# Performance work log

Hardware: AMD Instinct MI355X
Metric: run time of the kernel (lower is better)

Reference implementation:

```python
import jax, jax.numpy as jnp
import numpy as np

C = 64          # num_channels
DEPTH = 9       # dilation_depth
REPEAT = 2      # dilation_repeat
K = 2           # kernel_size
DILATIONS = [2 ** j for _ in range(REPEAT) for j in range(DEPTH)]
L = len(DILATIONS)  # 18 gated layers


def causal_conv(x, w, b, dilation):
    # x: [B, Cin, T], w: [Cout, Cin, K] -> [B, Cout, T] with causal (left) padding
    pad = (w.shape[-1] - 1) * dilation
    y = jax.lax.conv_general_dilated(
        x, w, window_strides=(1,), padding=[(pad, 0)],
        rhs_dilation=(dilation,), dimension_numbers=("NCH", "OIH", "NCH"))
    return y + b[None, :, None]


def setup_inputs() -> dict:
    key = jax.random.key(0)
    ks = jax.random.split(key, 9)
    s = 0.1
    x = jax.random.normal(ks[0], (4, 1, 65536), dtype=jnp.float32)
    in_w = jax.random.normal(ks[1], (C, 1, 1), dtype=jnp.float32) * s
    in_b = jax.random.normal(ks[2], (C,), dtype=jnp.float32) * s
    hid_w = jax.random.normal(ks[3], (L, 2 * C, C, K), dtype=jnp.float32) * s
    hid_b = jax.random.normal(ks[4], (L, 2 * C), dtype=jnp.float32) * s
    res_w = jax.random.normal(ks[5], (L, C, C, 1), dtype=jnp.float32) * s
    res_b = jax.random.normal(ks[6], (L, C), dtype=jnp.float32) * s
    mix_w = jax.random.normal(ks[7], (1, C * L, 1), dtype=jnp.float32) * s
    mix_b = jax.random.normal(ks[8], (1,), dtype=jnp.float32) * s
    return {"x": x, "in_w": in_w, "in_b": in_b, "hid_w": hid_w, "hid_b": hid_b,
            "res_w": res_w, "res_b": res_b, "mix_w": mix_w, "mix_b": mix_b}


def reference(x, in_w, in_b, hid_w, hid_b, res_w, res_b, mix_w, mix_b):
    # Input 1x1 conv: [B,1,T] -> [B,C,T]
    out = causal_conv(x, in_w, in_b, 1)
    skips = []
    for i, d in enumerate(DILATIONS):
        xi = out
        h = causal_conv(xi, hid_w[i], hid_b[i], d)       # [B, 2C, T]
        gated = jnp.tanh(h[:, :C]) * jax.nn.sigmoid(h[:, C:])  # [B, C, T]
        skips.append(gated)
        out = causal_conv(gated, res_w[i], res_b[i], 1) + xi    # residual
    skip = jnp.concatenate(skips, axis=1)                # [B, C*L, T]
    return causal_conv(skip, mix_w, mix_b, 1)            # [B, 1, T]
```

## Files before the change

### kernel.cpp

```cpp
#include <hip/hip_runtime.h>
#include <hip/hip_bf16.h>
#include <math.h>

#define NCH 64
#define T_LEN 65536
#define NLAYER 18

typedef __attribute__((ext_vector_type(8))) short bf16x8;
typedef __attribute__((ext_vector_type(4))) short bf16x4;
typedef __attribute__((ext_vector_type(4))) float f32x4;

static __device__ __forceinline__ float bf2f(short s) {
    union { short u[2]; float f; } v;
    v.u[0] = 0; v.u[1] = s;
    return v.f;
}
static __device__ __forceinline__ short f2bf(float f) {
    __hip_bfloat16 h = __float2bfloat16(f);
    return *(short*)&h;
}

__global__ void convert_weights_kernel(const float* __restrict__ hid_w,
                                       const float* __restrict__ res_w,
                                       __hip_bfloat16* __restrict__ whid,
                                       __hip_bfloat16* __restrict__ wres) {
    int gid = blockIdx.x * 256 + threadIdx.x;
    if (gid < NLAYER * 128 * 128) {
        int l   = gid >> 14;
        int rem = gid & 16383;
        int o   = rem >> 7;
        int k   = rem & 127;
        float v = (k < 64)
            ? hid_w[((l * 128 + o) * 64 + k) * 2]
            : hid_w[((l * 128 + o) * 64 + (k - 64)) * 2 + 1];
        whid[gid] = __float2bfloat16(v);
    }
    if (gid < NLAYER * 64 * 64) {
        wres[gid] = __float2bfloat16(res_w[gid]);
    }
}

__global__ __launch_bounds__(256, 3) void fused6_kernel(
    const void* __restrict__ src,
    __hip_bfloat16* __restrict__ next,
    float* __restrict__ acc,
    const __hip_bfloat16* __restrict__ whid_all,
    const float* __restrict__ hb_all,
    const __hip_bfloat16* __restrict__ wres_all,
    const float* __restrict__ rb_all,
    const float* __restrict__ mix_w,
    const float* __restrict__ in_w,
    const float* __restrict__ in_b,
    int lbase, int is_first) {
    __shared__ __align__(16) __hip_bfloat16 A[192 * 64];
    __shared__ __align__(16) __hip_bfloat16 G[192 * 64];

#define SW(row, col) ((row) * 64 + ((col) ^ (((row) & 7) << 3)))

    const int b    = blockIdx.x >> 9;
    const int widx = blockIdx.x & 511;
    const int t0   = widx << 7;
    const int tw   = t0 - 64;

    const int tid  = threadIdx.x;
    const int lane = tid & 63;
    const int w4   = tid >> 6;
    const int l15  = lane & 15;
    const int quad = lane >> 4;
    const int m0   = w4 * 16;
    const int rr   = tid >> 3;
    const int co   = (tid & 7) * 8;

    if (is_first) {
        const float* x = (const float*)src;
        float iw[8], ib[8];
#pragma unroll
        for (int j = 0; j < 8; ++j) { iw[j] = in_w[co + j]; ib[j] = in_b[co + j]; }
#pragma unroll
        for (int round = 0; round < 6; ++round) {
            int r  = round * 32 + rr;
            int gt = tw + r;
            bf16x8 v = {0, 0, 0, 0, 0, 0, 0, 0};
            if (gt >= 0) {
                float xv = x[(size_t)b * T_LEN + gt];
#pragma unroll
                for (int j = 0; j < 8; ++j) v[j] = f2bf(iw[j] * xv + ib[j]);
            }
            *(bf16x8*)(&A[SW(r, co)]) = v;
        }
    } else {
        const __hip_bfloat16* prev = (const __hip_bfloat16*)src;
#pragma unroll
        for (int round = 0; round < 6; ++round) {
            int r  = round * 32 + rr;
            int gt = tw + r;
            bf16x8 v = {0, 0, 0, 0, 0, 0, 0, 0};
            if (gt >= 0)
                v = *(const bf16x8*)(prev + ((size_t)b * T_LEN + gt) * NCH + co);
            *(bf16x8*)(&A[SW(r, co)]) = v;
        }
    }

    float skp[8] = {0.f, 0.f, 0.f, 0.f, 0.f, 0.f, 0.f, 0.f};

#pragma unroll 1
    for (int l = 0; l < 6; ++l) {
        const int d = 1 << l;
        const __hip_bfloat16* whid = whid_all + (size_t)(lbase + l) * 16384;
        const __hip_bfloat16* wres = wres_all + (size_t)(lbase + l) * 4096;
        const float* hb = hb_all + (lbase + l) * 128;
        const float* rb = rb_all + (lbase + l) * 64;
        const float* mw = mix_w + (lbase + l) * 64;

        bf16x8 aT[4], aS[4], aR[2];
        {
            const __hip_bfloat16* whT = whid + (size_t)(m0 + l15) * 128 + quad * 8;
            const __hip_bfloat16* whS = whT + 64 * 128;
#pragma unroll
            for (int k = 0; k < 4; ++k) {
                aT[k] = *(const bf16x8*)(whT + k * 32);
                aS[k] = *(const bf16x8*)(whS + k * 32);
            }
            const __hip_bfloat16* wrA = wres + (size_t)(m0 + l15) * 64 + quad * 8;
            aR[0] = *(const bf16x8*)(wrA);
            aR[1] = *(const bf16x8*)(wrA + 32);
        }
        f32x4 biasT, biasS, biasR;
#pragma unroll
        for (int r = 0; r < 4; ++r) {
            biasT[r] = hb[m0 + quad * 4 + r];
            biasS[r] = hb[64 + m0 + quad * 4 + r];
            biasR[r] = rb[m0 + quad * 4 + r];
        }
        f32x4 mw4 = *(const f32x4*)(mw + m0 + quad * 4);

        __syncthreads();

#pragma unroll
        for (int ct = 0; ct < 3; ++ct) {
            f32x4 accT[4], accS[4];
#pragma unroll
            for (int nt = 0; nt < 4; ++nt) { accT[nt] = biasT; accS[nt] = biasS; }
#pragma unroll
            for (int ks = 0; ks < 4; ++ks) {
                const int koff = (ks & 1) * 32 + quad * 8;
#pragma unroll
                for (int nt = 0; nt < 4; ++nt) {
                    int trow = ct * 64 + nt * 16 + l15;
                    int prow = trow - d;  prow = prow < 0 ? 0 : prow;
                    int row  = (ks < 2) ? prow : trow;
                    bf16x8 bx = *(const bf16x8*)(&A[SW(row, koff)]);
                    accT[nt] = __builtin_amdgcn_mfma_f32_16x16x32_bf16(aT[ks], bx, accT[nt], 0, 0, 0);
                    accS[nt] = __builtin_amdgcn_mfma_f32_16x16x32_bf16(aS[ks], bx, accS[nt], 0, 0, 0);
                }
            }
#pragma unroll
            for (int nt = 0; nt < 4; ++nt) {
                int trow = ct * 64 + nt * 16 + l15;
                bf16x4 gv;
                float gsum = 0.f;
#pragma unroll
                for (int r = 0; r < 4; ++r) {
                    float ea = __expf(2.f * accT[nt][r]);
                    float eb = __expf(-accS[nt][r]);
                    float g  = (ea - 1.f) *
                               __builtin_amdgcn_rcpf((ea + 1.f) * (1.f + eb));
                    gsum += mw4[r] * g;
                    gv[r] = f2bf(g);
                }
                if (ct >= 1) skp[(ct - 1) * 4 + nt] += gsum;
                *(bf16x4*)(&G[SW(trow, m0 + quad * 4)]) = gv;
            }
        }
        __syncthreads();

#pragma unroll
        for (int ct = 0; ct < 3; ++ct) {
            f32x4 accR[4];
#pragma unroll
            for (int nt = 0; nt < 4; ++nt) accR[nt] = biasR;
#pragma unroll
            for (int ks = 0; ks < 2; ++ks) {
                const int koff = ks * 32 + quad * 8;
#pragma unroll
                for (int nt = 0; nt < 4; ++nt) {
                    int trow = ct * 64 + nt * 16 + l15;
                    bf16x8 bx = *(const bf16x8*)(&G[SW(trow, koff)]);
                    accR[nt] = __builtin_amdgcn_mfma_f32_16x16x32_bf16(aR[ks], bx, accR[nt], 0, 0, 0);
                }
            }
#pragma unroll
            for (int nt = 0; nt < 4; ++nt) {
                int trow = ct * 64 + nt * 16 + l15;
                bf16x4 old = *(const bf16x4*)(&A[SW(trow, m0 + quad * 4)]);
                bool ok = (tw + trow) >= 0;
                bf16x4 ov;
#pragma unroll
                for (int r = 0; r < 4; ++r) {
                    float v = accR[nt][r] + bf2f(old[r]);
                    ov[r] = f2bf(ok ? v : 0.f);
                }
                *(bf16x4*)(&A[SW(trow, m0 + quad * 4)]) = ov;
            }
        }
    }
    __syncthreads();

#pragma unroll
    for (int round = 0; round < 4; ++round) {
        int pr = round * 32 + rr;
        *(bf16x8*)(next + ((size_t)b * T_LEN + t0 + pr) * NCH + co) =
            *(const bf16x8*)(&A[SW(pr + 64, co)]);
    }

    float* skbuf = (float*)G;
#pragma unroll
    for (int i = 0; i < 8; ++i) {
        skp[i] += __shfl_xor(skp[i], 16, 64);
        skp[i] += __shfl_xor(skp[i], 32, 64);
    }
    if (quad == 0) {
#pragma unroll
        for (int i = 0; i < 8; ++i) {
            int ct = i >> 2, nt = i & 3;
            skbuf[w4 * 128 + ct * 64 + nt * 16 + l15] = skp[i];
        }
    }
    __syncthreads();
    if (tid < 128) {
        float tot = skbuf[tid] + skbuf[128 + tid] +
                    skbuf[256 + tid] + skbuf[384 + tid];
        acc[(size_t)b * T_LEN + t0 + tid] += tot;
    }
#undef SW
}

__global__ __launch_bounds__(256, 2) void layer_mfma_kernel(
    const __hip_bfloat16* __restrict__ prev,
    __hip_bfloat16* __restrict__ next,
    float* __restrict__ acc,
    const __hip_bfloat16* __restrict__ whid,
    const float* __restrict__ hb,
    const __hip_bfloat16* __restrict__ wres,
    const float* __restrict__ rb,
    const float* __restrict__ mw,
    int d) {
    __shared__ __align__(16) __hip_bfloat16 Xp[64 * 72];
    __shared__ __align__(16) __hip_bfloat16 Xc[64 * 72];
    __shared__ __align__(16) __hip_bfloat16 Gt[64 * 72];

    const int t0   = blockIdx.x << 6;
    const int tid  = threadIdx.x;
    const int lane = tid & 63;
    const int w4   = tid >> 6;
    const int l15  = lane & 15;
    const int quad = lane >> 4;
    const int m0   = w4 * 16;
    const int rr = tid >> 3;
    const int co = (tid & 7) * 8;

    bf16x8 aT[4], aS[4], aR[2];
    {
        const __hip_bfloat16* whT = whid + (size_t)(m0 + l15) * 128 + quad * 8;
        const __hip_bfloat16* whS = whT + 64 * 128;
#pragma unroll
        for (int k = 0; k < 4; ++k) {
            aT[k] = *(const bf16x8*)(whT + k * 32);
            aS[k] = *(const bf16x8*)(whS + k * 32);
        }
        const __hip_bfloat16* wrA = wres + (size_t)(m0 + l15) * 64 + quad * 8;
        aR[0] = *(const bf16x8*)(wrA);
        aR[1] = *(const bf16x8*)(wrA + 32);
    }
    f32x4 biasT, biasS, biasR;
#pragma unroll
    for (int r = 0; r < 4; ++r) {
        biasT[r] = hb[m0 + quad * 4 + r];
        biasS[r] = hb[64 + m0 + quad * 4 + r];
        biasR[r] = rb[m0 + quad * 4 + r];
    }
    float mwq[16];
#pragma unroll
    for (int j = 0; j < 16; ++j) mwq[j] = mw[quad * 16 + j];

    bf16x8 pc[2], pp[2];
#define LOAD_TILE(b)                                                          \
    do {                                                                      \
        const __hip_bfloat16* pb = prev + ((size_t)(b) * T_LEN + t0) * NCH;   \
        _Pragma("unroll")                                                     \
        for (int pass = 0; pass < 2; ++pass) {                                \
            int r = pass * 32 + rr;                                           \
            pc[pass] = *(const bf16x8*)(pb + r * NCH + co);                   \
            int tp = t0 + r - d;                                              \
            bf16x8 z = {0, 0, 0, 0, 0, 0, 0, 0};                              \
            pp[pass] = z;                                                     \
            if (tp >= 0)                                                      \
                pp[pass] = *(const bf16x8*)(prev +                            \
                    ((size_t)(b) * T_LEN + tp) * NCH + co);                   \
        }                                                                     \
    } while (0)

    LOAD_TILE(0);

#pragma unroll
    for (int b = 0; b < 4; ++b) {
#pragma unroll
        for (int pass = 0; pass < 2; ++pass) {
            int r = pass * 32 + rr;
            *(bf16x8*)(&Xc[r * 72 + co]) = pc[pass];
            *(bf16x8*)(&Xp[r * 72 + co]) = pp[pass];
        }
        __syncthreads();

        if (b < 3) LOAD_TILE(b + 1);

        f32x4 accT[4], accS[4];
#pragma unroll
        for (int nt = 0; nt < 4; ++nt) { accT[nt] = biasT; accS[nt] = biasS; }
#pragma unroll
        for (int ks = 0; ks < 4; ++ks) {
            const __hip_bfloat16* srcb = (ks < 2) ? Xp : Xc;
            const int kk = (ks & 1) * 32 + quad * 8;
#pragma unroll
            for (int nt = 0; nt < 4; ++nt) {
                bf16x8 bx = *(const bf16x8*)(&srcb[(nt * 16 + l15) * 72 + kk]);
                accT[nt] = __builtin_amdgcn_mfma_f32_16x16x32_bf16(aT[ks], bx, accT[nt], 0, 0, 0);
                accS[nt] = __builtin_amdgcn_mfma_f32_16x16x32_bf16(aS[ks], bx, accS[nt], 0, 0, 0);
            }
        }

#pragma unroll
        for (int nt = 0; nt < 4; ++nt) {
            int t = nt * 16 + l15;
#pragma unroll
            for (int r = 0; r < 4; ++r) {
                float e2 = __expf(2.f * accT[nt][r]);
                float th = 1.f - 2.f * __builtin_amdgcn_rcpf(e2 + 1.f);
                float sg = __builtin_amdgcn_rcpf(1.f + __expf(-accS[nt][r]));
                Gt[t * 72 + m0 + quad * 4 + r] = __float2bfloat16(th * sg);
            }
        }

        bf16x4 curres[4];
#pragma unroll
        for (int nt = 0; nt < 4; ++nt) {
            curres[nt] = *(const bf16x4*)(&Xc[(nt * 16 + l15) * 72 + m0 + quad * 4]);
        }
        __syncthreads();

        f32x4 accR[4];
#pragma unroll
        for (int nt = 0; nt < 4; ++nt) accR[nt] = biasR;
#pragma unroll
        for (int ks = 0; ks < 2; ++ks) {
            const int kk = ks * 32 + quad * 8;
#pragma unroll
            for (int nt = 0; nt < 4; ++nt) {
                bf16x8 bx = *(const bf16x8*)(&Gt[(nt * 16 + l15) * 72 + kk]);
                accR[nt] = __builtin_amdgcn_mfma_f32_16x16x32_bf16(aR[ks], bx, accR[nt], 0, 0, 0);
            }
        }

        __hip_bfloat16* nb = next + ((size_t)b * T_LEN + t0) * NCH;
#pragma unroll
        for (int nt = 0; nt < 4; ++nt) {
            int t = nt * 16 + l15;
            bf16x4 ov;
#pragma unroll
            for (int r = 0; r < 4; ++r) {
                ov[r] = f2bf(accR[nt][r] + bf2f(curres[nt][r]));
            }
            *(bf16x4*)(nb + t * NCH + m0 + quad * 4) = ov;
        }

        {
            int t = w4 * 16 + l15;
            bf16x8 g0 = *(const bf16x8*)(&Gt[t * 72 + quad * 16]);
            bf16x8 g1 = *(const bf16x8*)(&Gt[t * 72 + quad * 16 + 8]);
            float s = 0.f;
#pragma unroll
            for (int j = 0; j < 8; ++j) {
                s += mwq[j]     * bf2f(g0[j]);
                s += mwq[8 + j] * bf2f(g1[j]);
            }
            s += __shfl_xor(s, 16, 64);
            s += __shfl_xor(s, 32, 64);
            if (quad == 0)
                acc[(size_t)b * T_LEN + t0 + t] += s;
        }
    }
#undef LOAD_TILE
}

__global__ __launch_bounds__(256, 2) void last_layer_kernel(
    const __hip_bfloat16* __restrict__ prev,
    const float* __restrict__ acc,
    float* __restrict__ out,
    const __hip_bfloat16* __restrict__ whid,
    const float* __restrict__ hb,
    const float* __restrict__ mw,
    const float* __restrict__ mix_b,
    int d) {
    __shared__ __align__(16) __hip_bfloat16 Xp[64 * 72];
    __shared__ __align__(16) __hip_bfloat16 Xc[64 * 72];
    __shared__ float skb[4 * 64];

    const int t0   = blockIdx.x << 6;
    const int tid  = threadIdx.x;
    const int lane = tid & 63;
    const int w4   = tid >> 6;
    const int l15  = lane & 15;
    const int quad = lane >> 4;
    const int m0   = w4 * 16;
    const int rr = tid >> 3;
    const int co = (tid & 7) * 8;

    bf16x8 aT[4], aS[4];
    {
        const __hip_bfloat16* whT = whid + (size_t)(m0 + l15) * 128 + quad * 8;
        const __hip_bfloat16* whS = whT + 64 * 128;
#pragma unroll
        for (int k = 0; k < 4; ++k) {
            aT[k] = *(const bf16x8*)(whT + k * 32);
            aS[k] = *(const bf16x8*)(whS + k * 32);
        }
    }
    f32x4 biasT, biasS;
    float mwv[4];
#pragma unroll
    for (int r = 0; r < 4; ++r) {
        biasT[r] = hb[m0 + quad * 4 + r];
        biasS[r] = hb[64 + m0 + quad * 4 + r];
        mwv[r]   = mw[m0 + quad * 4 + r];
    }
    const float mb = mix_b[0];

    bf16x8 pc[2], pp[2];
#define LOAD_TILE(b)                                                          \
    do {                                                                      \
        const __hip_bfloat16* pb = prev + ((size_t)(b) * T_LEN + t0) * NCH;   \
        _Pragma("unroll")                                                     \
        for (int pass = 0; pass < 2; ++pass) {                                \
            int r = pass * 32 + rr;                                           \
            pc[pass] = *(const bf16x8*)(pb + r * NCH + co);                   \
            int tp = t0 + r - d;                                              \
            bf16x8 z = {0, 0, 0, 0, 0, 0, 0, 0};                              \
            pp[pass] = z;                                                     \
            if (tp >= 0)                                                      \
                pp[pass] = *(const bf16x8*)(prev +                            \
                    ((size_t)(b) * T_LEN + tp) * NCH + co);                   \
        }                                                                     \
    } while (0)

    LOAD_TILE(0);

#pragma unroll
    for (int b = 0; b < 4; ++b) {
#pragma unroll
        for (int pass = 0; pass < 2; ++pass) {
            int r = pass * 32 + rr;
            *(bf16x8*)(&Xc[r * 72 + co]) = pc[pass];
            *(bf16x8*)(&Xp[r * 72 + co]) = pp[pass];
        }
        __syncthreads();

        if (b < 3) LOAD_TILE(b + 1);

        f32x4 accT[4], accS[4];
#pragma unroll
        for (int nt = 0; nt < 4; ++nt) { accT[nt] = biasT; accS[nt] = biasS; }
#pragma unroll
        for (int ks = 0; ks < 4; ++ks) {
            const __hip_bfloat16* srcb = (ks < 2) ? Xp : Xc;
            const int kk = (ks & 1) * 32 + quad * 8;
#pragma unroll
            for (int nt = 0; nt < 4; ++nt) {
                bf16x8 bx = *(const bf16x8*)(&srcb[(nt * 16 + l15) * 72 + kk]);
                accT[nt] = __builtin_amdgcn_mfma_f32_16x16x32_bf16(aT[ks], bx, accT[nt], 0, 0, 0);
                accS[nt] = __builtin_amdgcn_mfma_f32_16x16x32_bf16(aS[ks], bx, accS[nt], 0, 0, 0);
            }
        }

#pragma unroll
        for (int nt = 0; nt < 4; ++nt) {
            float sv = 0.f;
#pragma unroll
            for (int r = 0; r < 4; ++r) {
                float e2 = __expf(2.f * accT[nt][r]);
                float th = 1.f - 2.f * __builtin_amdgcn_rcpf(e2 + 1.f);
                float sg = __builtin_amdgcn_rcpf(1.f + __expf(-accS[nt][r]));
                sv += mwv[r] * (th * sg);
            }
            sv += __shfl_xor(sv, 16, 64);
            sv += __shfl_xor(sv, 32, 64);
            if (quad == 0)
                skb[w4 * 64 + nt * 16 + l15] = sv;
        }
        __syncthreads();

        if (tid < 64) {
            float tot = skb[tid] + skb[64 + tid] + skb[128 + tid] + skb[192 + tid];
            out[(size_t)b * T_LEN + t0 + tid] =
                acc[(size_t)b * T_LEN + t0 + tid] + tot + mb;
        }
    }
#undef LOAD_TILE
}

extern "C" void kernel_launch(void* const* d_in, const int* in_sizes, int n_in,
                              void* d_out, int out_size, void* d_ws, size_t ws_size,
                              hipStream_t stream) {
    const float* x     = (const float*)d_in[0];
    const float* in_w  = (const float*)d_in[1];
    const float* in_b  = (const float*)d_in[2];
    const float* hid_w = (const float*)d_in[3];
    const float* hid_b = (const float*)d_in[4];
    const float* res_w = (const float*)d_in[5];
    const float* res_b = (const float*)d_in[6];
    const float* mix_w = (const float*)d_in[7];
    const float* mix_b = (const float*)d_in[8];
    float* out = (float*)d_out;

    const size_t act_elems = 4ull * T_LEN * NCH;
    __hip_bfloat16* actA = (__hip_bfloat16*)d_ws;
    __hip_bfloat16* actB = actA + act_elems;
    float* acc = (float*)(actB + act_elems);
    __hip_bfloat16* whid = (__hip_bfloat16*)(acc + 4ull * T_LEN);
    __hip_bfloat16* wres = whid + (size_t)NLAYER * 128 * 128;

    hipMemsetAsync(acc, 0, 4ull * T_LEN * sizeof(float), stream);

    convert_weights_kernel<<<1152, 256, 0, stream>>>(hid_w, res_w, whid, wres);

    fused6_kernel<<<2048, 256, 0, stream>>>(
        x, actA, acc, whid, hid_b, wres, res_b, mix_w, in_w, in_b, 0, 1);

    layer_mfma_kernel<<<1024, 256, 0, stream>>>(
        actA, actB, acc, whid + 6 * 16384, hid_b + 6 * 128,
        wres + 6 * 4096, res_b + 6 * 64, mix_w + 6 * 64, 64);
    layer_mfma_kernel<<<1024, 256, 0, stream>>>(
        actB, actA, acc, whid + 7 * 16384, hid_b + 7 * 128,
        wres + 7 * 4096, res_b + 7 * 64, mix_w + 7 * 64, 128);
    layer_mfma_kernel<<<1024, 256, 0, stream>>>(
        actA, actB, acc, whid + 8 * 16384, hid_b + 8 * 128,
        wres + 8 * 4096, res_b + 8 * 64, mix_w + 8 * 64, 256);

    fused6_kernel<<<2048, 256, 0, stream>>>(
        actB, actA, acc, whid, hid_b, wres, res_b, mix_w, in_w, in_b, 9, 0);

    layer_mfma_kernel<<<1024, 256, 0, stream>>>(
        actA, actB, acc, whid + 15 * 16384, hid_b + 15 * 128,
        wres + 15 * 4096, res_b + 15 * 64, mix_w + 15 * 64, 64);
    layer_mfma_kernel<<<1024, 256, 0, stream>>>(
        actB, actA, acc, whid + 16 * 16384, hid_b + 16 * 128,
        wres + 16 * 4096, res_b + 16 * 64, mix_w + 16 * 64, 128);

    last_layer_kernel<<<1024, 256, 0, stream>>>(
        actA, acc, out, whid + 17 * 16384, hid_b + 17 * 128,
        mix_w + 17 * 64, mix_b, 256);
}
```

Measured before the change: 530.4 us.

## Split fused6 work across 8 waves and raise occupancy bounds on layer kernels

The fused six-layer kernel now runs 512 threads per block. Each of 8 waves covers a 16-channel group for half of the 192 time rows, so it holds 3 accumulator tiles per chunk instead of 4 tiles over 3 chunks. This lowers per-wave register pressure and doubles the waves available to hide LDS and MFMA latency for the same shared-memory tile. The skip-sum bookkeeping is remapped to match. Separately, launch bounds on layer_mfma_kernel and last_layer_kernel are raised to 4 blocks per CU, which may force register spills.

After: 1.245 ms. 2.35x slower.

```diff
diff --git a/kernel.cpp b/kernel.cpp
--- a/kernel.cpp
+++ b/kernel.cpp
@@ -40,7 +40,7 @@
     }
 }
 
-__global__ __launch_bounds__(256, 3) void fused6_kernel(
+__global__ __launch_bounds__(512, 6) void fused6_kernel(
     const void* __restrict__ src,
     __hip_bfloat16* __restrict__ next,
     float* __restrict__ acc,
@@ -64,10 +64,13 @@
 
     const int tid  = threadIdx.x;
     const int lane = tid & 63;
-    const int w4   = tid >> 6;
+    const int w8   = tid >> 6;
+    const int rh   = w8 >> 2;
+    const int cg   = w8 & 3;
     const int l15  = lane & 15;
     const int quad = lane >> 4;
-    const int m0   = w4 * 16;
+    const int m0   = cg * 16;
+    const int rbase = rh * 96;
     const int rr   = tid >> 3;
     const int co   = (tid & 7) * 8;
 
@@ -77,8 +80,8 @@
 #pragma unroll
         for (int j = 0; j < 8; ++j) { iw[j] = in_w[co + j]; ib[j] = in_b[co + j]; }
 #pragma unroll
-        for (int round = 0; round < 6; ++round) {
-            int r  = round * 32 + rr;
+        for (int round = 0; round < 3; ++round) {
+            int r  = round * 64 + rr;
             int gt = tw + r;
             bf16x8 v = {0, 0, 0, 0, 0, 0, 0, 0};
             if (gt >= 0) {
@@ -91,8 +94,8 @@
     } else {
         const __hip_bfloat16* prev = (const __hip_bfloat16*)src;
 #pragma unroll
-        for (int round = 0; round < 6; ++round) {
-            int r  = round * 32 + rr;
+        for (int round = 0; round < 3; ++round) {
+            int r  = round * 64 + rr;
             int gt = tw + r;
             bf16x8 v = {0, 0, 0, 0, 0, 0, 0, 0};
             if (gt >= 0)
@@ -101,7 +104,7 @@
         }
     }
 
-    float skp[8] = {0.f, 0.f, 0.f, 0.f, 0.f, 0.f, 0.f, 0.f};
+    float skp[6] = {0.f, 0.f, 0.f, 0.f, 0.f, 0.f};
 
 #pragma unroll 1
     for (int l = 0; l < 6; ++l) {
@@ -137,16 +140,16 @@
         __syncthreads();
 
 #pragma unroll
-        for (int ct = 0; ct < 3; ++ct) {
-            f32x4 accT[4], accS[4];
-#pragma unroll
-            for (int nt = 0; nt < 4; ++nt) { accT[nt] = biasT; accS[nt] = biasS; }
+        for (int ch = 0; ch < 2; ++ch) {
+            f32x4 accT[3], accS[3];
+#pragma unroll
+            for (int nt = 0; nt < 3; ++nt) { accT[nt] = biasT; accS[nt] = biasS; }
 #pragma unroll
             for (int ks = 0; ks < 4; ++ks) {
                 const int koff = (ks & 1) * 32 + quad * 8;
 #pragma unroll
-                for (int nt = 0; nt < 4; ++nt) {
-                    int trow = ct * 64 + nt * 16 + l15;
+                for (int nt = 0; nt < 3; ++nt) {
+                    int trow = rbase + ch * 48 + nt * 16 + l15;
                     int prow = trow - d;  prow = prow < 0 ? 0 : prow;
                     int row  = (ks < 2) ? prow : trow;
                     bf16x8 bx = *(const bf16x8*)(&A[SW(row, koff)]);
@@ -155,8 +158,8 @@
                 }
             }
 #pragma unroll
-            for (int nt = 0; nt < 4; ++nt) {
-                int trow = ct * 64 + nt * 16 + l15;
+            for (int nt = 0; nt < 3; ++nt) {
+                int trow = rbase + ch * 48 + nt * 16 + l15;
                 bf16x4 gv;
                 float gsum = 0.f;
 #pragma unroll
@@ -168,30 +171,31 @@
                     gsum += mw4[r] * g;
                     gv[r] = f2bf(g);
                 }
-                if (ct >= 1) skp[(ct - 1) * 4 + nt] += gsum;
+                if (rh == 1 || ch * 48 + nt * 16 >= 64)
+                    skp[ch * 3 + nt] += gsum;
                 *(bf16x4*)(&G[SW(trow, m0 + quad * 4)]) = gv;
             }
         }
         __syncthreads();
 
 #pragma unroll
-        for (int ct = 0; ct < 3; ++ct) {
-            f32x4 accR[4];
-#pragma unroll
-            for (int nt = 0; nt < 4; ++nt) accR[nt] = biasR;
+        for (int ch = 0; ch < 2; ++ch) {
+            f32x4 accR[3];
+#pragma unroll
+            for (int nt = 0; nt < 3; ++nt) accR[nt] = biasR;
 #pragma unroll
             for (int ks = 0; ks < 2; ++ks) {
                 const int koff = ks * 32 + quad * 8;
 #pragma unroll
-                for (int nt = 0; nt < 4; ++nt) {
-                    int trow = ct * 64 + nt * 16 + l15;
+                for (int nt = 0; nt < 3; ++nt) {
+                    int trow = rbase + ch * 48 + nt * 16 + l15;
                     bf16x8 bx = *(const bf16x8*)(&G[SW(trow, koff)]);
                     accR[nt] = __builtin_amdgcn_mfma_f32_16x16x32_bf16(aR[ks], bx, accR[nt], 0, 0, 0);
                 }
             }
 #pragma unroll
-            for (int nt = 0; nt < 4; ++nt) {
-                int trow = ct * 64 + nt * 16 + l15;
+            for (int nt = 0; nt < 3; ++nt) {
+                int trow = rbase + ch * 48 + nt * 16 + l15;
                 bf16x4 old = *(const bf16x4*)(&A[SW(trow, m0 + quad * 4)]);
                 bool ok = (tw + trow) >= 0;
                 bf16x4 ov;
@@ -207,23 +211,28 @@
     __syncthreads();
 
 #pragma unroll
-    for (int round = 0; round < 4; ++round) {
-        int pr = round * 32 + rr;
+    for (int round = 0; round < 2; ++round) {
+        int pr = round * 64 + rr;
         *(bf16x8*)(next + ((size_t)b * T_LEN + t0 + pr) * NCH + co) =
             *(const bf16x8*)(&A[SW(pr + 64, co)]);
     }
 
     float* skbuf = (float*)G;
 #pragma unroll
-    for (int i = 0; i < 8; ++i) {
+    for (int i = 0; i < 6; ++i) {
         skp[i] += __shfl_xor(skp[i], 16, 64);
         skp[i] += __shfl_xor(skp[i], 32, 64);
     }
     if (quad == 0) {
 #pragma unroll
-        for (int i = 0; i < 8; ++i) {
-            int ct = i >> 2, nt = i & 3;
-            skbuf[w4 * 128 + ct * 64 + nt * 16 + l15] = skp[i];
+        for (int ch = 0; ch < 2; ++ch) {
+#pragma unroll
+            for (int nt = 0; nt < 3; ++nt) {
+                if (rh == 1 || ch * 48 + nt * 16 >= 64) {
+                    int row = rbase + ch * 48 + nt * 16 + l15 - 64;
+                    skbuf[cg * 128 + row] = skp[ch * 3 + nt];
+                }
+            }
         }
     }
     __syncthreads();
@@ -235,7 +244,7 @@
 #undef SW
 }
 
-__global__ __launch_bounds__(256, 2) void layer_mfma_kernel(
+__global__ __launch_bounds__(256, 4) void layer_mfma_kernel(
     const __hip_bfloat16* __restrict__ prev,
     __hip_bfloat16* __restrict__ next,
     float* __restrict__ acc,
@@ -392,7 +401,7 @@
 #undef LOAD_TILE
 }
 
-__global__ __launch_bounds__(256, 2) void last_layer_kernel(
+__global__ __launch_bounds__(256, 4) void last_layer_kernel(
     const __hip_bfloat16* __restrict__ prev,
     const float* __restrict__ acc,
     float* __restrict__ out,
@@ -532,7 +541,7 @@
 
     convert_weights_kernel<<<1152, 256, 0, stream>>>(hid_w, res_w, whid, wres);
 
-    fused6_kernel<<<2048, 256, 0, stream>>>(
+    fused6_kernel<<<2048, 512, 0, stream>>>(
         x, actA, acc, whid, hid_b, wres, res_b, mix_w, in_w, in_b, 0, 1);
 
     layer_mfma_kernel<<<1024, 256, 0, stream>>>(
@@ -545,7 +554,7 @@
         actA, actB, acc, whid + 8 * 16384, hid_b + 8 * 128,
         wres + 8 * 4096, res_b + 8 * 64, mix_w + 8 * 64, 256);
 
-    fused6_kernel<<<2048, 256, 0, stream>>>(
+    fused6_kernel<<<2048, 512, 0, stream>>>(
         actB, actA, acc, whid, hid_b, wres, res_b, mix_w, in_w, in_b, 9, 0);
 
     layer_mfma_kernel<<<1024, 256, 0, stream>>>(
```

## Double-buffer gate tile and interleave gated and residual GEMMs per chunk

Applied to the files above, without the earlier changes.

The full 192-row gate buffer in the fused six-layer kernel is replaced by two 64-row slots. The gated GEMM for one 64-row chunk is now interleaved with the residual GEMM of the previous chunk, and residual writes back into A are deferred past barriers to avoid read/write hazards. The smaller shared-memory footprint allows the launch bound to rise from 3 to 4 blocks per CU, aiming at more latency hiding. In exchange, more values stay live in registers (saved old activations and epilogue tiles) under a tighter per-thread register budget, which could cause spills.

Result: slower. 718.2 us (+35.4%).

```diff
diff --git a/kernel.cpp b/kernel.cpp
--- a/kernel.cpp
+++ b/kernel.cpp
@@ -40,7 +40,7 @@
     }
 }
 
-__global__ __launch_bounds__(256, 3) void fused6_kernel(
+__global__ __launch_bounds__(256, 4) void fused6_kernel(
     const void* __restrict__ src,
     __hip_bfloat16* __restrict__ next,
     float* __restrict__ acc,
@@ -53,7 +53,7 @@
     const float* __restrict__ in_b,
     int lbase, int is_first) {
     __shared__ __align__(16) __hip_bfloat16 A[192 * 64];
-    __shared__ __align__(16) __hip_bfloat16 G[192 * 64];
+    __shared__ __align__(16) __hip_bfloat16 Gb[2][64 * 64];
 
 #define SW(row, col) ((row) * 64 + ((col) ^ (((row) & 7) << 3)))
 
@@ -103,6 +103,72 @@
 
     float skp[8] = {0.f, 0.f, 0.f, 0.f, 0.f, 0.f, 0.f, 0.f};
 
+#define GEMM1_GATE(ct, slot)                                                  \
+    do {                                                                      \
+        f32x4 accT[4], accS[4];                                               \
+        _Pragma("unroll")                                                     \
+        for (int nt = 0; nt < 4; ++nt) { accT[nt] = biasT; accS[nt] = biasS; }\
+        _Pragma("unroll")                                                     \
+        for (int ks = 0; ks < 4; ++ks) {                                      \
+            const int koff = (ks & 1) * 32 + quad * 8;                        \
+            _Pragma("unroll")                                                 \
+            for (int nt = 0; nt < 4; ++nt) {                                  \
+                int trow = (ct) * 64 + nt * 16 + l15;                         \
+                int prow = trow - d;  prow = prow < 0 ? 0 : prow;             \
+                int row  = (ks < 2) ? prow : trow;                            \
+                bf16x8 bx = *(const bf16x8*)(&A[SW(row, koff)]);              \
+                accT[nt] = __builtin_amdgcn_mfma_f32_16x16x32_bf16(           \
+                    aT[ks], bx, accT[nt], 0, 0, 0);                           \
+                accS[nt] = __builtin_amdgcn_mfma_f32_16x16x32_bf16(           \
+                    aS[ks], bx, accS[nt], 0, 0, 0);                           \
+            }                                                                 \
+        }                                                                     \
+        _Pragma("unroll")                                                     \
+        for (int nt = 0; nt < 4; ++nt) {                                      \
+            bf16x4 gv;                                                        \
+            float gsum = 0.f;                                                 \
+            _Pragma("unroll")                                                 \
+            for (int r = 0; r < 4; ++r) {                                     \
+                float ea = __expf(2.f * accT[nt][r]);                         \
+                float eb = __expf(-accS[nt][r]);                              \
+                float g  = (ea - 1.f) *                                       \
+                           __builtin_amdgcn_rcpf((ea + 1.f) * (1.f + eb));    \
+                gsum += mw4[r] * g;                                           \
+                gv[r] = f2bf(g);                                              \
+            }                                                                 \
+            if ((ct) >= 1) skp[((ct) - 1) * 4 + nt] += gsum;                  \
+            *(bf16x4*)(&Gb[slot][SW(nt * 16 + l15, m0 + quad * 4)]) = gv;     \
+        }                                                                     \
+    } while (0)
+
+#define GEMM2_EPI(ct, slot, aold, epi)                                        \
+    do {                                                                      \
+        f32x4 accR[4];                                                        \
+        _Pragma("unroll")                                                     \
+        for (int nt = 0; nt < 4; ++nt) accR[nt] = biasR;                      \
+        _Pragma("unroll")                                                     \
+        for (int ks = 0; ks < 2; ++ks) {                                      \
+            const int koff = ks * 32 + quad * 8;                              \
+            _Pragma("unroll")                                                 \
+            for (int nt = 0; nt < 4; ++nt) {                                  \
+                bf16x8 bx =                                                   \
+                    *(const bf16x8*)(&Gb[slot][SW(nt * 16 + l15, koff)]);     \
+                accR[nt] = __builtin_amdgcn_mfma_f32_16x16x32_bf16(           \
+                    aR[ks], bx, accR[nt], 0, 0, 0);                           \
+            }                                                                 \
+        }                                                                     \
+        _Pragma("unroll")                                                     \
+        for (int nt = 0; nt < 4; ++nt) {                                      \
+            int trow = (ct) * 64 + nt * 16 + l15;                             \
+            bool ok = (tw + trow) >= 0;                                       \
+            _Pragma("unroll")                                                 \
+            for (int r = 0; r < 4; ++r) {                                     \
+                float v = accR[nt][r] + bf2f(aold[nt][r]);                    \
+                epi[nt][r] = f2bf(ok ? v : 0.f);                              \
+            }                                                                 \
+        }                                                                     \
+    } while (0)
+
 #pragma unroll 1
     for (int l = 0; l < 6; ++l) {
         const int d = 1 << l;
@@ -136,72 +202,39 @@
 
         __syncthreads();
 
-#pragma unroll
-        for (int ct = 0; ct < 3; ++ct) {
-            f32x4 accT[4], accS[4];
-#pragma unroll
-            for (int nt = 0; nt < 4; ++nt) { accT[nt] = biasT; accS[nt] = biasS; }
-#pragma unroll
-            for (int ks = 0; ks < 4; ++ks) {
-                const int koff = (ks & 1) * 32 + quad * 8;
-#pragma unroll
-                for (int nt = 0; nt < 4; ++nt) {
-                    int trow = ct * 64 + nt * 16 + l15;
-                    int prow = trow - d;  prow = prow < 0 ? 0 : prow;
-                    int row  = (ks < 2) ? prow : trow;
-                    bf16x8 bx = *(const bf16x8*)(&A[SW(row, koff)]);
-                    accT[nt] = __builtin_amdgcn_mfma_f32_16x16x32_bf16(aT[ks], bx, accT[nt], 0, 0, 0);
-                    accS[nt] = __builtin_amdgcn_mfma_f32_16x16x32_bf16(aS[ks], bx, accS[nt], 0, 0, 0);
-                }
-            }
-#pragma unroll
-            for (int nt = 0; nt < 4; ++nt) {
-                int trow = ct * 64 + nt * 16 + l15;
-                bf16x4 gv;
-                float gsum = 0.f;
-#pragma unroll
-                for (int r = 0; r < 4; ++r) {
-                    float ea = __expf(2.f * accT[nt][r]);
-                    float eb = __expf(-accS[nt][r]);
-                    float g  = (ea - 1.f) *
-                               __builtin_amdgcn_rcpf((ea + 1.f) * (1.f + eb));
-                    gsum += mw4[r] * g;
-                    gv[r] = f2bf(g);
-                }
-                if (ct >= 1) skp[(ct - 1) * 4 + nt] += gsum;
-                *(bf16x4*)(&G[SW(trow, m0 + quad * 4)]) = gv;
-            }
-        }
-        __syncthreads();
-
-#pragma unroll
-        for (int ct = 0; ct < 3; ++ct) {
-            f32x4 accR[4];
-#pragma unroll
-            for (int nt = 0; nt < 4; ++nt) accR[nt] = biasR;
-#pragma unroll
-            for (int ks = 0; ks < 2; ++ks) {
-                const int koff = ks * 32 + quad * 8;
-#pragma unroll
-                for (int nt = 0; nt < 4; ++nt) {
-                    int trow = ct * 64 + nt * 16 + l15;
-                    bf16x8 bx = *(const bf16x8*)(&G[SW(trow, koff)]);
-                    accR[nt] = __builtin_amdgcn_mfma_f32_16x16x32_bf16(aR[ks], bx, accR[nt], 0, 0, 0);
-                }
-            }
-#pragma unroll
-            for (int nt = 0; nt < 4; ++nt) {
-                int trow = ct * 64 + nt * 16 + l15;
-                bf16x4 old = *(const bf16x4*)(&A[SW(trow, m0 + quad * 4)]);
-                bool ok = (tw + trow) >= 0;
-                bf16x4 ov;
-#pragma unroll
-                for (int r = 0; r < 4; ++r) {
-                    float v = accR[nt][r] + bf2f(old[r]);
-                    ov[r] = f2bf(ok ? v : 0.f);
-                }
-                *(bf16x4*)(&A[SW(trow, m0 + quad * 4)]) = ov;
-            }
+        GEMM1_GATE(0, 0);
+        __syncthreads();
+
+        bf16x4 aold0[4], aold2[4], epi0[4];
+        GEMM1_GATE(1, 1);
+#pragma unroll
+        for (int nt = 0; nt < 4; ++nt) {
+            aold0[nt] = *(const bf16x4*)(&A[SW(nt * 16 + l15, m0 + quad * 4)]);
+            aold2[nt] = *(const bf16x4*)(&A[SW(128 + nt * 16 + l15, m0 + quad * 4)]);
+        }
+        GEMM2_EPI(0, 0, aold0, epi0);
+        __syncthreads();
+
+#pragma unroll
+        for (int nt = 0; nt < 4; ++nt)
+            *(bf16x4*)(&A[SW(nt * 16 + l15, m0 + quad * 4)]) = epi0[nt];
+        {
+            bf16x4 aold1[4], epi1[4];
+            GEMM1_GATE(2, 0);
+#pragma unroll
+            for (int nt = 0; nt < 4; ++nt)
+                aold1[nt] = *(const bf16x4*)(&A[SW(64 + nt * 16 + l15, m0 + quad * 4)]);
+            GEMM2_EPI(1, 1, aold1, epi1);
+            __syncthreads();
+
+#pragma unroll
+            for (int nt = 0; nt < 4; ++nt)
+                *(bf16x4*)(&A[SW(64 + nt * 16 + l15, m0 + quad * 4)]) = epi1[nt];
+            bf16x4 epi2[4];
+            GEMM2_EPI(2, 0, aold2, epi2);
+#pragma unroll
+            for (int nt = 0; nt < 4; ++nt)
+                *(bf16x4*)(&A[SW(128 + nt * 16 + l15, m0 + quad * 4)]) = epi2[nt];
         }
     }
     __syncthreads();
@@ -213,7 +246,7 @@
             *(const bf16x8*)(&A[SW(pr + 64, co)]);
     }
 
-    float* skbuf = (float*)G;
+    float* skbuf = (float*)Gb;
 #pragma unroll
     for (int i = 0; i < 8; ++i) {
         skp[i] += __shfl_xor(skp[i], 16, 64);
@@ -233,6 +266,8 @@
         acc[(size_t)b * T_LEN + t0 + tid] += tot;
     }
 #undef SW
+#undef GEMM1_GATE
+#undef GEMM2_EPI
 }
 
 __global__ __launch_bounds__(256, 2) void layer_mfma_kernel(
```

## Cut register pressure in layer kernel to raise occupancy to three blocks

Applied to the files above, without the earlier changes.

The per-layer MFMA kernel now targets three blocks per CU instead of two. It removes the register prefetch of the next batch tile, splits the gated-conv accumulation into two halves of two N-tiles each, and reloads residual weights and bias per batch iteration instead of keeping them resident. The skip-sum now comes from the fp32 gate values times per-row mix weights, reduced across waves through a small shared buffer, rather than re-reading bf16 gates from LDS. The tanh·sigmoid is also merged to use a single reciprocal. In exchange, it gives up overlap of global loads with compute, adds repeated weight loads, and adds an extra shared-memory stage.

Result: no change. 528.5 us (-0.4%).

```diff
diff --git a/kernel.cpp b/kernel.cpp
--- a/kernel.cpp
+++ b/kernel.cpp
@@ -235,7 +235,7 @@
 #undef SW
 }
 
-__global__ __launch_bounds__(256, 2) void layer_mfma_kernel(
+__global__ __launch_bounds__(256, 3) void layer_mfma_kernel(
     const __hip_bfloat16* __restrict__ prev,
     __hip_bfloat16* __restrict__ next,
     float* __restrict__ acc,
@@ -248,6 +248,7 @@
     __shared__ __align__(16) __hip_bfloat16 Xp[64 * 72];
     __shared__ __align__(16) __hip_bfloat16 Xc[64 * 72];
     __shared__ __align__(16) __hip_bfloat16 Gt[64 * 72];
+    __shared__ float skb[4 * 64];
 
     const int t0   = blockIdx.x << 6;
     const int tid  = threadIdx.x;
@@ -259,7 +260,7 @@
     const int rr = tid >> 3;
     const int co = (tid & 7) * 8;
 
-    bf16x8 aT[4], aS[4], aR[2];
+    bf16x8 aT[4], aS[4];
     {
         const __hip_bfloat16* whT = whid + (size_t)(m0 + l15) * 128 + quad * 8;
         const __hip_bfloat16* whS = whT + 64 * 128;
@@ -268,20 +269,170 @@
             aT[k] = *(const bf16x8*)(whT + k * 32);
             aS[k] = *(const bf16x8*)(whS + k * 32);
         }
-        const __hip_bfloat16* wrA = wres + (size_t)(m0 + l15) * 64 + quad * 8;
-        aR[0] = *(const bf16x8*)(wrA);
-        aR[1] = *(const bf16x8*)(wrA + 32);
-    }
-    f32x4 biasT, biasS, biasR;
+    }
+    f32x4 biasT, biasS;
 #pragma unroll
     for (int r = 0; r < 4; ++r) {
         biasT[r] = hb[m0 + quad * 4 + r];
         biasS[r] = hb[64 + m0 + quad * 4 + r];
-        biasR[r] = rb[m0 + quad * 4 + r];
-    }
-    float mwq[16];
-#pragma unroll
-    for (int j = 0; j < 16; ++j) mwq[j] = mw[quad * 16 + j];
+    }
+    f32x4 mw4 = *(const f32x4*)(mw + m0 + quad * 4);
+
+#pragma unroll 1
+    for (int b = 0; b < 4; ++b) {
+        {
+            const __hip_bfloat16* pb = prev + ((size_t)b * T_LEN + t0) * NCH;
+#pragma unroll
+            for (int pass = 0; pass < 2; ++pass) {
+                int r = pass * 32 + rr;
+                bf16x8 vc = *(const bf16x8*)(pb + r * NCH + co);
+                int tp = t0 + r - d;
+                bf16x8 vp = {0, 0, 0, 0, 0, 0, 0, 0};
+                if (tp >= 0)
+                    vp = *(const bf16x8*)(prev + ((size_t)b * T_LEN + tp) * NCH + co);
+                *(bf16x8*)(&Xc[r * 72 + co]) = vc;
+                *(bf16x8*)(&Xp[r * 72 + co]) = vp;
+            }
+        }
+        __syncthreads();
+
+        float sk[4];
+#pragma unroll
+        for (int np = 0; np < 2; ++np) {
+            f32x4 accT[2], accS[2];
+#pragma unroll
+            for (int h = 0; h < 2; ++h) { accT[h] = biasT; accS[h] = biasS; }
+#pragma unroll
+            for (int ks = 0; ks < 4; ++ks) {
+                const __hip_bfloat16* srcb = (ks < 2) ? Xp : Xc;
+                const int kk = (ks & 1) * 32 + quad * 8;
+#pragma unroll
+                for (int h = 0; h < 2; ++h) {
+                    int nt = np * 2 + h;
+                    bf16x8 bx = *(const bf16x8*)(&srcb[(nt * 16 + l15) * 72 + kk]);
+                    accT[h] = __builtin_amdgcn_mfma_f32_16x16x32_bf16(aT[ks], bx, accT[h], 0, 0, 0);
+                    accS[h] = __builtin_amdgcn_mfma_f32_16x16x32_bf16(aS[ks], bx, accS[h], 0, 0, 0);
+                }
+            }
+#pragma unroll
+            for (int h = 0; h < 2; ++h) {
+                int nt = np * 2 + h;
+                float gsum = 0.f;
+#pragma unroll
+                for (int r = 0; r < 4; ++r) {
+                    float ea = __expf(2.f * accT[h][r]);
+                    float eb = __expf(-accS[h][r]);
+                    float g  = (ea - 1.f) *
+                               __builtin_amdgcn_rcpf((ea + 1.f) * (1.f + eb));
+                    gsum += mw4[r] * g;
+                    Gt[(nt * 16 + l15) * 72 + m0 + quad * 4 + r] = __float2bfloat16(g);
+                }
+                sk[nt] = gsum;
+            }
+        }
+#pragma unroll
+        for (int nt = 0; nt < 4; ++nt) {
+            sk[nt] += __shfl_xor(sk[nt], 16, 64);
+            sk[nt] += __shfl_xor(sk[nt], 32, 64);
+        }
+        if (quad == 0) {
+#pragma unroll
+            for (int nt = 0; nt < 4; ++nt)
+                skb[w4 * 64 + nt * 16 + l15] = sk[nt];
+        }
+
+        bf16x4 curres[4];
+#pragma unroll
+        for (int nt = 0; nt < 4; ++nt) {
+            curres[nt] = *(const bf16x4*)(&Xc[(nt * 16 + l15) * 72 + m0 + quad * 4]);
+        }
+        __syncthreads();
+
+        bf16x8 aR0, aR1;
+        {
+            const __hip_bfloat16* wrA = wres + (size_t)(m0 + l15) * 64 + quad * 8;
+            aR0 = *(const bf16x8*)(wrA);
+            aR1 = *(const bf16x8*)(wrA + 32);
+        }
+        f32x4 biasR;
+#pragma unroll
+        for (int r = 0; r < 4; ++r) biasR[r] = rb[m0 + quad * 4 + r];
+
+        f32x4 accR[4];
+#pragma unroll
+        for (int nt = 0; nt < 4; ++nt) accR[nt] = biasR;
+#pragma unroll
+        for (int ks = 0; ks < 2; ++ks) {
+            const int kk = ks * 32 + quad * 8;
+#pragma unroll
+            for (int nt = 0; nt < 4; ++nt) {
+                bf16x8 bx = *(const bf16x8*)(&Gt[(nt * 16 + l15) * 72 + kk]);
+                accR[nt] = __builtin_amdgcn_mfma_f32_16x16x32_bf16(
+                    (ks == 0) ? aR0 : aR1, bx, accR[nt], 0, 0, 0);
+            }
+        }
+
+        __hip_bfloat16* nb = next + ((size_t)b * T_LEN + t0) * NCH;
+#pragma unroll
+        for (int nt = 0; nt < 4; ++nt) {
+            int t = nt * 16 + l15;
+            bf16x4 ov;
+#pragma unroll
+            for (int r = 0; r < 4; ++r) {
+                ov[r] = f2bf(accR[nt][r] + bf2f(curres[nt][r]));
+            }
+            *(bf16x4*)(nb + t * NCH + m0 + quad * 4) = ov;
+        }
+
+        if (tid < 64) {
+            float tot = skb[tid] + skb[64 + tid] + skb[128 + tid] + skb[192 + tid];
+            acc[(size_t)b * T_LEN + t0 + tid] += tot;
+        }
+    }
+}
+
+__global__ __launch_bounds__(256, 2) void last_layer_kernel(
+    const __hip_bfloat16* __restrict__ prev,
+    const float* __restrict__ acc,
+    float* __restrict__ out,
+    const __hip_bfloat16* __restrict__ whid,
+    const float* __restrict__ hb,
+    const float* __restrict__ mw,
+    const float* __restrict__ mix_b,
+    int d) {
+    __shared__ __align__(16) __hip_bfloat16 Xp[64 * 72];
+    __shared__ __align__(16) __hip_bfloat16 Xc[64 * 72];
+    __shared__ float skb[4 * 64];
+
+    const int t0   = blockIdx.x << 6;
+    const int tid  = threadIdx.x;
+    const int lane = tid & 63;
+    const int w4   = tid >> 6;
+    const int l15  = lane & 15;
+    const int quad = lane >> 4;
+    const int m0   = w4 * 16;
+    const int rr = tid >> 3;
+    const int co = (tid & 7) * 8;
+
+    bf16x8 aT[4], aS[4];
+    {
+        const __hip_bfloat16* whT = whid + (size_t)(m0 + l15) * 128 + quad * 8;
+        const __hip_bfloat16* whS = whT + 64 * 128;
+#pragma unroll
+        for (int k = 0; k < 4; ++k) {
+            aT[k] = *(const bf16x8*)(whT + k * 32);
+            aS[k] = *(const bf16x8*)(whS + k * 32);
+        }
+    }
+    f32x4 biasT, biasS;
+    float mwv[4];
+#pragma unroll
+    for (int r = 0; r < 4; ++r) {
+        biasT[r] = hb[m0 + quad * 4 + r];
+        biasS[r] = hb[64 + m0 + quad * 4 + r];
+        mwv[r]   = mw[m0 + quad * 4 + r];
+    }
+    const float mb = mix_b[0];
 
     bf16x8 pc[2], pp[2];
 #define LOAD_TILE(b)                                                          \
@@ -331,158 +482,6 @@
 
 #pragma unroll
         for (int nt = 0; nt < 4; ++nt) {
-            int t = nt * 16 + l15;
-#pragma unroll
-            for (int r = 0; r < 4; ++r) {
-                float e2 = __expf(2.f * accT[nt][r]);
-                float th = 1.f - 2.f * __builtin_amdgcn_rcpf(e2 + 1.f);
-                float sg = __builtin_amdgcn_rcpf(1.f + __expf(-accS[nt][r]));
-                Gt[t * 72 + m0 + quad * 4 + r] = __float2bfloat16(th * sg);
-            }
-        }
-
-        bf16x4 curres[4];
-#pragma unroll
-        for (int nt = 0; nt < 4; ++nt) {
-            curres[nt] = *(const bf16x4*)(&Xc[(nt * 16 + l15) * 72 + m0 + quad * 4]);
-        }
-        __syncthreads();
-
-        f32x4 accR[4];
-#pragma unroll
-        for (int nt = 0; nt < 4; ++nt) accR[nt] = biasR;
-#pragma unroll
-        for (int ks = 0; ks < 2; ++ks) {
-            const int kk = ks * 32 + quad * 8;
-#pragma unroll
-            for (int nt = 0; nt < 4; ++nt) {
-                bf16x8 bx = *(const bf16x8*)(&Gt[(nt * 16 + l15) * 72 + kk]);
-                accR[nt] = __builtin_amdgcn_mfma_f32_16x16x32_bf16(aR[ks], bx, accR[nt], 0, 0, 0);
-            }
-        }
-
-        __hip_bfloat16* nb = next + ((size_t)b * T_LEN + t0) * NCH;
-#pragma unroll
-        for (int nt = 0; nt < 4; ++nt) {
-            int t = nt * 16 + l15;
-            bf16x4 ov;
-#pragma unroll
-            for (int r = 0; r < 4; ++r) {
-                ov[r] = f2bf(accR[nt][r] + bf2f(curres[nt][r]));
-            }
-            *(bf16x4*)(nb + t * NCH + m0 + quad * 4) = ov;
-        }
-
-        {
-            int t = w4 * 16 + l15;
-            bf16x8 g0 = *(const bf16x8*)(&Gt[t * 72 + quad * 16]);
-            bf16x8 g1 = *(const bf16x8*)(&Gt[t * 72 + quad * 16 + 8]);
-            float s = 0.f;
-#pragma unroll
-            for (int j = 0; j < 8; ++j) {
-                s += mwq[j]     * bf2f(g0[j]);
-                s += mwq[8 + j] * bf2f(g1[j]);
-            }
-            s += __shfl_xor(s, 16, 64);
-            s += __shfl_xor(s, 32, 64);
-            if (quad == 0)
-                acc[(size_t)b * T_LEN + t0 + t] += s;
-        }
-    }
-#undef LOAD_TILE
-}
-
-__global__ __launch_bounds__(256, 2) void last_layer_kernel(
-    const __hip_bfloat16* __restrict__ prev,
-    const float* __restrict__ acc,
-    float* __restrict__ out,
-    const __hip_bfloat16* __restrict__ whid,
-    const float* __restrict__ hb,
-    const float* __restrict__ mw,
-    const float* __restrict__ mix_b,
-    int d) {
-    __shared__ __align__(16) __hip_bfloat16 Xp[64 * 72];
-    __shared__ __align__(16) __hip_bfloat16 Xc[64 * 72];
-    __shared__ float skb[4 * 64];
-
-    const int t0   = blockIdx.x << 6;
-    const int tid  = threadIdx.x;
-    const int lane = tid & 63;
-    const int w4   = tid >> 6;
-    const int l15  = lane & 15;
-    const int quad = lane >> 4;
-    const int m0   = w4 * 16;
-    const int rr = tid >> 3;
-    const int co = (tid & 7) * 8;
-
-    bf16x8 aT[4], aS[4];
-    {
-        const __hip_bfloat16* whT = whid + (size_t)(m0 + l15) * 128 + quad * 8;
-        const __hip_bfloat16* whS = whT + 64 * 128;
-#pragma unroll
-        for (int k = 0; k < 4; ++k) {
-            aT[k] = *(const bf16x8*)(whT + k * 32);
-            aS[k] = *(const bf16x8*)(whS + k * 32);
-        }
-    }
-    f32x4 biasT, biasS;
-    float mwv[4];
-#pragma unroll
-    for (int r = 0; r < 4; ++r) {
-        biasT[r] = hb[m0 + quad * 4 + r];
-        biasS[r] = hb[64 + m0 + quad * 4 + r];
-        mwv[r]   = mw[m0 + quad * 4 + r];
-    }
-    const float mb = mix_b[0];
-
-    bf16x8 pc[2], pp[2];
-#define LOAD_TILE(b)                                                          \
-    do {                                                                      \
-        const __hip_bfloat16* pb = prev + ((size_t)(b) * T_LEN + t0) * NCH;   \
-        _Pragma("unroll")                                                     \
-        for (int pass = 0; pass < 2; ++pass) {                                \
-            int r = pass * 32 + rr;                                           \
-            pc[pass] = *(const bf16x8*)(pb + r * NCH + co);                   \
-            int tp = t0 + r - d;                                              \
-            bf16x8 z = {0, 0, 0, 0, 0, 0, 0, 0};                              \
-            pp[pass] = z;                                                     \
-            if (tp >= 0)                                                      \
-                pp[pass] = *(const bf16x8*)(prev +                            \
-                    ((size_t)(b) * T_LEN + tp) * NCH + co);                   \
-        }                                                                     \
-    } while (0)
-
-    LOAD_TILE(0);
-
-#pragma unroll
-    for (int b = 0; b < 4; ++b) {
-#pragma unroll
-        for (int pass = 0; pass < 2; ++pass) {
-            int r = pass * 32 + rr;
-            *(bf16x8*)(&Xc[r * 72 + co]) = pc[pass];
-            *(bf16x8*)(&Xp[r * 72 + co]) = pp[pass];
-        }
-        __syncthreads();
-
-        if (b < 3) LOAD_TILE(b + 1);
-
-        f32x4 accT[4], accS[4];
-#pragma unroll
-        for (int nt = 0; nt < 4; ++nt) { accT[nt] = biasT; accS[nt] = biasS; }
-#pragma unroll
-        for (int ks = 0; ks < 4; ++ks) {
-            const __hip_bfloat16* srcb = (ks < 2) ? Xp : Xc;
-            const int kk = (ks & 1) * 32 + quad * 8;
-#pragma unroll
-            for (int nt = 0; nt < 4; ++nt) {
-                bf16x8 bx = *(const bf16x8*)(&srcb[(nt * 16 + l15) * 72 + kk]);
-                accT[nt] = __builtin_amdgcn_mfma_f32_16x16x32_bf16(aT[ks], bx, accT[nt], 0, 0, 0);
-                accS[nt] = __builtin_amdgcn_mfma_f32_16x16x32_bf16(aS[ks], bx, accS[nt], 0, 0, 0);
-            }
-        }
-
-#pragma unroll
-        for (int nt = 0; nt < 4; ++nt) {
             float sv = 0.f;
 #pragma unroll
             for (int r = 0; r < 4; ++r) {
```
